# Kernel tuning notes

Hardware: AMD Instinct MI355X
Metric: run time of the kernel (lower is better)

Reference implementation:

```python
import jax, jax.numpy as jnp
import numpy as np

MARGIN = 0.1

def setup_inputs() -> dict:
    key = jax.random.key(0)
    k1, k2 = jax.random.split(key)
    embeddings = jax.random.normal(k1, (8192, 128), dtype=jnp.float32)
    labels = jax.random.randint(k2, (8192,), 0, 64, dtype=jnp.int64)
    return {"embeddings": embeddings, "labels": labels}

def reference(embeddings, labels):
    # sim[i,j] = <e_i, e_j>
    sim = embeddings @ embeddings.T  # [n, n]
    eq = labels[:, None] == labels[None, :]  # pos mask (includes diagonal)
    # per entry: exp(margin - sim) for positives, exp(sim - margin) for negatives
    terms = jnp.where(eq, jnp.exp(MARGIN - sim), jnp.exp(sim - MARGIN))
    # loss_i = log(sum_j terms[i,j]); loss = mean_i loss_i
    return jnp.mean(jnp.log(jnp.sum(terms, axis=1)))
```

## Files before the change

### kernel.cpp

```cpp
#include <hip/hip_runtime.h>
#include <hip/hip_bf16.h>

#define N 8192
#define D 128
#define LOG2E  1.44269504088896f
#define MLOG2E 0.14426950408890f
#define LN2    0.69314718055995f

#define COLSB   272
#define NSTEPS  8

typedef __attribute__((ext_vector_type(8))) short bf16x8;
typedef __attribute__((ext_vector_type(4))) float f32x4;

#if __has_builtin(__builtin_amdgcn_exp2f)
#define EXP2(x) __builtin_amdgcn_exp2f(x)
#else
#define EXP2(x) exp2f(x)
#endif
#if __has_builtin(__builtin_amdgcn_logf)
#define LOG2(x) __builtin_amdgcn_logf(x)
#else
#define LOG2(x) log2f(x)
#endif

static __device__ __forceinline__ unsigned short f2bf(float f) {
    union { float f; unsigned int u; } x;
    x.f = f;
    unsigned int r = ((x.u >> 16) & 1u) + 0x7FFFu;
    return (unsigned short)((x.u + r) >> 16);
}

__global__ void prep_kernel(const float* __restrict__ E,
                            unsigned short* __restrict__ Eb,
                            float* __restrict__ rowsum,
                            float* __restrict__ out) {
    int idx = blockIdx.x * 256 + threadIdx.x;
    float4 v = ((const float4*)E)[idx];
    ushort4 o;
    o.x = f2bf(v.x); o.y = f2bf(v.y); o.z = f2bf(v.z); o.w = f2bf(v.w);
    ((ushort4*)Eb)[idx] = o;
    if (idx < N) rowsum[idx] = 0.0f;
    if (idx == 0) out[0] = 0.0f;
}

__global__ __launch_bounds__(256) void fused_kernel(
        const unsigned short* __restrict__ Eb,
        const int* __restrict__ labels,
        float* __restrict__ rowsum) {
    __shared__ __align__(16) char ldsbuf[2][32 * COLSB];

    const int tid  = threadIdx.x;
    const int wid  = tid >> 6;
    const int lane = tid & 63;
    const int cchunk = blockIdx.x & 31;
    const int rgroup = blockIdx.x >> 5;
    const int m0 = rgroup * 256 + wid * 64;
    const int n_begin = cchunk * 256;
    const int q = lane >> 4;
    const int l = lane & 15;

    bf16x8 a[4][4];
#pragma unroll
    for (int g = 0; g < 4; ++g) {
        const bf16x8* p = (const bf16x8*)(Eb + (size_t)(m0 + g * 16 + l) * D + q * 8);
#pragma unroll
        for (int kk = 0; kk < 4; ++kk) a[g][kk] = p[kk * 4];
    }

    int lrow[16];
#pragma unroll
    for (int g = 0; g < 4; ++g)
#pragma unroll
        for (int r = 0; r < 4; ++r)
            lrow[g * 4 + r] = labels[m0 + g * 16 + q * 4 + r];

    float sum[16];
#pragma unroll
    for (int i = 0; i < 16; ++i) sum[i] = 0.0f;

    const char* gB = (const char*)Eb + (size_t)n_begin * 256;
    const int gofs = tid * 32;
    const int lofs = (tid >> 3) * COLSB + (tid & 7) * 32;

    float4 v0, v1;
    {
        const float4* p = (const float4*)(gB + gofs);
        v0 = p[0]; v1 = p[1];
        float4* dst = (float4*)(&ldsbuf[0][lofs]);
        dst[0] = v0; dst[1] = v1;
        const float4* p1 = (const float4*)(gB + 32 * 256 + gofs);
        v0 = p1[0]; v1 = p1[1];
    }
    __syncthreads();

#pragma clang loop unroll(disable)
    for (int t = 0; t < NSTEPS; ++t) {
        if (t + 1 < NSTEPS) {
            float4* dst = (float4*)(&ldsbuf[(t + 1) & 1][lofs]);
            dst[0] = v0; dst[1] = v1;
        }
        if (t + 2 < NSTEPS) {
            const float4* p = (const float4*)(gB + (size_t)(t + 2) * 32 * 256 + gofs);
            v0 = p[0]; v1 = p[1];
        }

#pragma unroll
        for (int s = 0; s < 2; ++s) {
            const int col = n_begin + t * 32 + s * 16 + l;
            const int lc = labels[col];
            const char* lb = &ldsbuf[t & 1][(s * 16 + l) * COLSB + q * 16];
            bf16x8 b0 = *(const bf16x8*)(lb);
            bf16x8 b1 = *(const bf16x8*)(lb + 64);
            bf16x8 b2 = *(const bf16x8*)(lb + 128);
            bf16x8 b3 = *(const bf16x8*)(lb + 192);

            f32x4 acc[4];
#pragma unroll
            for (int g = 0; g < 4; ++g) {
                acc[g] = (f32x4){0.f, 0.f, 0.f, 0.f};
                acc[g] = __builtin_amdgcn_mfma_f32_16x16x32_bf16(a[g][0], b0, acc[g], 0, 0, 0);
                acc[g] = __builtin_amdgcn_mfma_f32_16x16x32_bf16(a[g][1], b1, acc[g], 0, 0, 0);
                acc[g] = __builtin_amdgcn_mfma_f32_16x16x32_bf16(a[g][2], b2, acc[g], 0, 0, 0);
                acc[g] = __builtin_amdgcn_mfma_f32_16x16x32_bf16(a[g][3], b3, acc[g], 0, 0, 0);
            }

#pragma unroll
            for (int g = 0; g < 4; ++g) {
#pragma unroll
                for (int r = 0; r < 4; ++r) {
                    float sv = acc[g][r];
                    bool eq = (lrow[g * 4 + r] == lc);
                    float c = eq ? -LOG2E : LOG2E;
                    float d = eq ? MLOG2E : -MLOG2E;
                    sum[g * 4 + r] += EXP2(fmaf(sv, c, d));
                }
            }
        }
        __syncthreads();
    }

#pragma unroll
    for (int i = 0; i < 16; ++i) {
        float v = sum[i];
        v += __shfl_xor(v, 1);
        v += __shfl_xor(v, 2);
        v += __shfl_xor(v, 4);
        v += __shfl_xor(v, 8);
        sum[i] = v;
    }
    if (l == 0) {
#pragma unroll
        for (int g = 0; g < 4; ++g)
#pragma unroll
            for (int r = 0; r < 4; ++r)
                atomicAdd(&rowsum[m0 + g * 16 + q * 4 + r], sum[g * 4 + r]);
    }
}

__global__ void finalize_kernel(const float* __restrict__ rowsum, float* __restrict__ out) {
    __shared__ float red[4];
    int i = blockIdx.x * 256 + threadIdx.x;
    float v = LOG2(rowsum[i]) * LN2;
#pragma unroll
    for (int off = 1; off <= 32; off <<= 1) v += __shfl_xor(v, off);
    if ((threadIdx.x & 63) == 0) red[threadIdx.x >> 6] = v;
    __syncthreads();
    if (threadIdx.x == 0)
        atomicAdd(out, (red[0] + red[1] + red[2] + red[3]) * (1.0f / (float)N));
}

extern "C" void kernel_launch(void* const* d_in, const int* in_sizes, int n_in,
                              void* d_out, int out_size, void* d_ws, size_t ws_size,
                              hipStream_t stream) {
    const float* E = (const float*)d_in[0];
    const int* labels = (const int*)d_in[1];
    float* out = (float*)d_out;

    unsigned short* Eb = (unsigned short*)d_ws;
    float* rowsum = (float*)((char*)d_ws + (size_t)N * D * sizeof(unsigned short));

    prep_kernel<<<1024, 256, 0, stream>>>(E, Eb, rowsum, out);
    fused_kernel<<<1024, 256, 0, stream>>>(Eb, labels, rowsum);
    finalize_kernel<<<32, 256, 0, stream>>>(rowsum, out);
}
```

Measured before the change: 96.68 us.

## Exploit similarity matrix symmetry by computing only upper-triangular tiles

The fused kernel now launches one block per upper-triangular 128x128 tile, 2080 blocks of 128 threads, and maps each block index to a (row, column) tile pair. Off-diagonal tiles also reduce each column's terms across the wave and atomically add them into that column's row sum, because the sim matrix and the label mask are both symmetric. This roughly halves the MFMA and exp work. In exchange it adds many more atomics on rowsum and a triangular index calculation, and it uses smaller blocks that each load a wider tile.

New measurement: 99.15 us. +2.6%, slower.

```diff
diff --git a/kernel.cpp b/kernel.cpp
--- a/kernel.cpp
+++ b/kernel.cpp
@@ -4,11 +4,10 @@
 #define N 8192
 #define D 128
 #define LOG2E  1.44269504088896f
-#define MLOG2E 0.14426950408890f
 #define LN2    0.69314718055995f
 
 #define COLSB   272
-#define NSTEPS  8
+#define NSTEPS  4
 
 typedef __attribute__((ext_vector_type(8))) short bf16x8;
 typedef __attribute__((ext_vector_type(4))) float f32x4;
@@ -44,7 +43,7 @@
     if (idx == 0) out[0] = 0.0f;
 }
 
-__global__ __launch_bounds__(256) void fused_kernel(
+__global__ __launch_bounds__(128) void fused_kernel(
         const unsigned short* __restrict__ Eb,
         const int* __restrict__ labels,
         float* __restrict__ rowsum) {
@@ -53,12 +52,17 @@
     const int tid  = threadIdx.x;
     const int wid  = tid >> 6;
     const int lane = tid & 63;
-    const int cchunk = blockIdx.x & 31;
-    const int rgroup = blockIdx.x >> 5;
-    const int m0 = rgroup * 256 + wid * 64;
-    const int n_begin = cchunk * 256;
     const int q = lane >> 4;
     const int l = lane & 15;
+
+    const int b = blockIdx.x;
+    int r = (int)(64.5f - sqrtf(64.5f * 64.5f - 2.0f * (float)b));
+    while ((r + 1) * 64 - ((r + 1) * r) / 2 <= b) ++r;
+    while (r * 64 - (r * (r - 1)) / 2 > b) --r;
+    const int c = r + (b - (r * 64 - (r * (r - 1)) / 2));
+    const bool diag = (r == c);
+    const int m0 = r * 128 + wid * 64;
+    const int n_begin = c * 128;
 
     bf16x8 a[4][4];
 #pragma unroll
@@ -72,25 +76,25 @@
 #pragma unroll
     for (int g = 0; g < 4; ++g)
 #pragma unroll
-        for (int r = 0; r < 4; ++r)
-            lrow[g * 4 + r] = labels[m0 + g * 16 + q * 4 + r];
+        for (int rr = 0; rr < 4; ++rr)
+            lrow[g * 4 + rr] = labels[m0 + g * 16 + q * 4 + rr];
 
     float sum[16];
 #pragma unroll
     for (int i = 0; i < 16; ++i) sum[i] = 0.0f;
 
     const char* gB = (const char*)Eb + (size_t)n_begin * 256;
-    const int gofs = tid * 32;
-    const int lofs = (tid >> 3) * COLSB + (tid & 7) * 32;
+    const int gofs = tid * 64;
+    const int lofs = (tid >> 2) * COLSB + (tid & 3) * 64;
 
-    float4 v0, v1;
+    float4 v0, v1, v2, v3;
     {
         const float4* p = (const float4*)(gB + gofs);
-        v0 = p[0]; v1 = p[1];
+        v0 = p[0]; v1 = p[1]; v2 = p[2]; v3 = p[3];
         float4* dst = (float4*)(&ldsbuf[0][lofs]);
-        dst[0] = v0; dst[1] = v1;
+        dst[0] = v0; dst[1] = v1; dst[2] = v2; dst[3] = v3;
         const float4* p1 = (const float4*)(gB + 32 * 256 + gofs);
-        v0 = p1[0]; v1 = p1[1];
+        v0 = p1[0]; v1 = p1[1]; v2 = p1[2]; v3 = p1[3];
     }
     __syncthreads();
 
@@ -98,11 +102,11 @@
     for (int t = 0; t < NSTEPS; ++t) {
         if (t + 1 < NSTEPS) {
             float4* dst = (float4*)(&ldsbuf[(t + 1) & 1][lofs]);
-            dst[0] = v0; dst[1] = v1;
+            dst[0] = v0; dst[1] = v1; dst[2] = v2; dst[3] = v3;
         }
         if (t + 2 < NSTEPS) {
             const float4* p = (const float4*)(gB + (size_t)(t + 2) * 32 * 256 + gofs);
-            v0 = p[0]; v1 = p[1];
+            v0 = p[0]; v1 = p[1]; v2 = p[2]; v3 = p[3];
         }
 
 #pragma unroll
@@ -125,16 +129,23 @@
                 acc[g] = __builtin_amdgcn_mfma_f32_16x16x32_bf16(a[g][3], b3, acc[g], 0, 0, 0);
             }
 
+            float cp = 0.0f;
 #pragma unroll
             for (int g = 0; g < 4; ++g) {
 #pragma unroll
-                for (int r = 0; r < 4; ++r) {
-                    float sv = acc[g][r];
-                    bool eq = (lrow[g * 4 + r] == lc);
-                    float c = eq ? -LOG2E : LOG2E;
-                    float d = eq ? MLOG2E : -MLOG2E;
-                    sum[g * 4 + r] += EXP2(fmaf(sv, c, d));
+                for (int rr = 0; rr < 4; ++rr) {
+                    float sv = acc[g][rr];
+                    bool eq = (lrow[g * 4 + rr] == lc);
+                    float cc = eq ? -LOG2E : LOG2E;
+                    float term = EXP2(cc * (sv - 0.1f));
+                    sum[g * 4 + rr] += term;
+                    cp += term;
                 }
+            }
+            if (!diag) {
+                cp += __shfl_xor(cp, 16);
+                cp += __shfl_xor(cp, 32);
+                if (q == 0) atomicAdd(&rowsum[col], cp);
             }
         }
         __syncthreads();
@@ -153,8 +164,8 @@
 #pragma unroll
         for (int g = 0; g < 4; ++g)
 #pragma unroll
-            for (int r = 0; r < 4; ++r)
-                atomicAdd(&rowsum[m0 + g * 16 + q * 4 + r], sum[g * 4 + r]);
+            for (int rr = 0; rr < 4; ++rr)
+                atomicAdd(&rowsum[m0 + g * 16 + q * 4 + rr], sum[g * 4 + rr]);
     }
 }
 
@@ -181,6 +192,6 @@
     float* rowsum = (float*)((char*)d_ws + (size_t)N * D * sizeof(unsigned short));
 
     prep_kernel<<<1024, 256, 0, stream>>>(E, Eb, rowsum, out);
-    fused_kernel<<<1024, 256, 0, stream>>>(Eb, labels, rowsum);
+    fused_kernel<<<2080, 128, 0, stream>>>(Eb, labels, rowsum);
     finalize_kernel<<<32, 256, 0, stream>>>(rowsum, out);
 }
```
